# Performance work log

Measured on AMD Instinct MI355X. Metric: run time of the kernel, lower is better.

## Reference

```python
import jax, jax.numpy as jnp
import numpy as np

L, S, D, H, DL, V, B = 8, 1024, 768, 12, 64, 512, 8
NB, NM = 32, 64  # big_bird neighbours, global memory columns


def _bigbird_mask():
    i = np.arange(S)[:, None]
    j = np.arange(S)[None, :]
    m = ((np.abs(i - j) <= NB) | (j < NM)) & (j <= i)  # window + global cols, then tril
    return jnp.asarray(m)[None, None]  # [1,1,S,S]


def _ln(x, g, b):
    mu = x.mean(-1, keepdims=True)
    var = ((x - mu) ** 2).mean(-1, keepdims=True)
    return (x - mu) / jnp.sqrt(var + 1e-5) * g + b


def setup_inputs() -> dict:
    key = jax.random.key(0)
    ks = jax.random.split(key, 16)
    s = 0.02
    d = {
        'x': jax.random.randint(ks[0], (B, S), 0, V),
        'targets': jax.random.randint(ks[1], (B, S), 0, V),
        'wte': jax.random.normal(ks[2], (V, D), jnp.float32) * s,
        'pos': jnp.zeros((1, S, D), jnp.float32),
        'ln1_g': jnp.ones((L, D)), 'ln1_b': jnp.zeros((L, D)),
        'wq': jax.random.normal(ks[3], (L, D, D)) * s, 'bq': jnp.zeros((L, D)),
        'wk': jax.random.normal(ks[4], (L, D, D)) * s, 'bk': jnp.zeros((L, D)),
        'wv': jax.random.normal(ks[5], (L, D, D)) * s, 'bv': jnp.zeros((L, D)),
        'ln2_g': jnp.ones((L, D)), 'ln2_b': jnp.zeros((L, D)),
        'w1': jax.random.normal(ks[6], (L, D, 4 * D)) * s, 'b1': jnp.zeros((L, 4 * D)),
        'w2': jax.random.normal(ks[7], (L, 4 * D, D)) * s, 'b2': jnp.zeros((L, D)),
        'lnf_g': jnp.ones((D,)), 'lnf_b': jnp.zeros((D,)),
        'w_out': jax.random.normal(ks[8], (D, V)) * s,
    }
    return d


def _forward(x, targets, wte, pos, ln1_g, ln1_b, wq, bq, wk, bk, wv, bv,
             ln2_g, ln2_b, w1, b1, w2, b2, lnf_g, lnf_b, w_out):
    mask = _bigbird_mask()
    h = wte[x] + pos  # [B,S,D]
    scale = DL ** -0.5
    neg_inf = jnp.array(float('-inf'), h.dtype)
    for l in range(L):
        a = _ln(h, ln1_g[l], ln1_b[l])
        q = (a @ wq[l] + bq[l]).reshape(B, S, H, DL).transpose(0, 2, 1, 3)
        k = (a @ wk[l] + bk[l]).reshape(B, S, H, DL).transpose(0, 2, 1, 3)
        v = (a @ wv[l] + bv[l]).reshape(B, S, H, DL).transpose(0, 2, 1, 3)
        att = jnp.einsum('bhqd,bhkd->bhqk', q, k) * scale
        att = jnp.where(mask, att, neg_inf)
        att = jax.nn.softmax(att, axis=-1)
        z = jnp.einsum('bhqk,bhkd->bhqd', att, v)
        z = z.transpose(0, 2, 1, 3).reshape(B, S, D)
        h = h + z  # note: W_0 is defined in the torch module but never applied
        m = _ln(h, ln2_g[l], ln2_b[l])
        h = h + jax.nn.gelu(m @ w1[l] + b1[l], approximate=False) @ w2[l] + b2[l]
    h = _ln(h, lnf_g, lnf_b)
    pred = h @ w_out  # [B,S,V]
    logp = jax.nn.log_softmax(pred.reshape(B * S, V), axis=-1)
    loss = -jnp.take_along_axis(logp, targets.reshape(-1, 1), axis=1).mean()
    return pred, loss


def reference(x, targets, wte, pos, ln1_g, ln1_b, wq, bq, wk, bk, wv, bv,
              ln2_g, ln2_b, w1, b1, w2, b2, lnf_g, lnf_b, w_out):
    return _forward(x, targets, wte, pos, ln1_g, ln1_b, wq, bq, wk, bk, wv, bv,
                    ln2_g, ln2_b, w1, b1, w2, b2, lnf_g, lnf_b, w_out)
```

## Files before the change

### kernel.cpp

```cpp
#include <hip/hip_runtime.h>
#include <hip/hip_bf16.h>

#define DEV __device__ __forceinline__

typedef __attribute__((ext_vector_type(8))) short short8;
typedef __attribute__((ext_vector_type(4))) float f32x4;

DEV unsigned short f2bf(float f){
  unsigned int u = __builtin_bit_cast(unsigned int, f);
  u += 0x7FFFu + ((u >> 16) & 1u);
  return (unsigned short)(u >> 16);
}

DEV void gld_lds16(const void* g, void* l){
  __builtin_amdgcn_global_load_lds((const __attribute__((address_space(1))) void*)g,
                                   (__attribute__((address_space(3))) void*)l, 16, 0, 0);
}

__global__ void k_embed(const int* __restrict__ x, const float* __restrict__ wte,
                        const float* __restrict__ pos, float* __restrict__ h){
  int i = blockIdx.x * 256 + threadIdx.x;
  int row = i / 768, d = i - row * 768;
  int s = row & 1023;
  h[i] = wte[x[row] * 768 + d] + pos[s * 768 + d];
}

__global__ void k_ln(const float* __restrict__ src, const float* __restrict__ g,
                     const float* __restrict__ b, unsigned short* __restrict__ out){
  int row = blockIdx.x, t = threadIdx.x;
  const float* p = src + (size_t)row * 768;
  float v0 = p[t], v1 = p[t + 256], v2 = p[t + 512];
  float s = v0 + v1 + v2;
  float sq = v0 * v0 + v1 * v1 + v2 * v2;
  #pragma unroll
  for(int m = 32; m >= 1; m >>= 1){ s += __shfl_xor(s, m); sq += __shfl_xor(sq, m); }
  __shared__ float red[8];
  int w = t >> 6;
  if((t & 63) == 0){ red[w] = s; red[4 + w] = sq; }
  __syncthreads();
  float S  = red[0] + red[1] + red[2] + red[3];
  float SQ = red[4] + red[5] + red[6] + red[7];
  float mu  = S * (1.0f / 768.0f);
  float var = SQ * (1.0f / 768.0f) - mu * mu;
  float inv = rsqrtf(var + 1e-5f);
  unsigned short* o = out + (size_t)row * 768;
  o[t]       = f2bf((v0 - mu) * inv * g[t]       + b[t]);
  o[t + 256] = f2bf((v1 - mu) * inv * g[t + 256] + b[t + 256]);
  o[t + 512] = f2bf((v2 - mu) * inv * g[t + 512] + b[t + 512]);
}

DEV void tr_tile(float (*tl)[33], const float* __restrict__ src, unsigned short* __restrict__ dst,
                 int R, int C, int tx, int ty, int tid){
  int lx = tid & 31, ly = tid >> 5;
  int r0 = ty * 32, c0 = tx * 32;
  #pragma unroll
  for(int i = 0; i < 4; i++) tl[ly + 8*i][lx] = src[(size_t)(r0 + ly + 8*i) * C + (c0 + lx)];
  __syncthreads();
  #pragma unroll
  for(int i = 0; i < 4; i++) dst[(size_t)(c0 + ly + 8*i) * R + (r0 + lx)] = f2bf(tl[lx][ly + 8*i]);
}

__global__ void k_convert_all(const float* __restrict__ wq, const float* __restrict__ wk,
                              const float* __restrict__ wv, const float* __restrict__ w1,
                              const float* __restrict__ w2, const float* __restrict__ bq,
                              const float* __restrict__ bk, const float* __restrict__ bv,
                              unsigned short* __restrict__ wall, float* __restrict__ qkvb,
                              int l0){
  __shared__ float tl[32][33];
  int l = l0 + blockIdx.y, slot = blockIdx.y;
  int bid = blockIdx.x, tid = threadIdx.x;
  unsigned short* wqkv_t = wall + (size_t)slot * 6488064;
  unsigned short* w1_t   = wqkv_t + 1769472;
  unsigned short* w2_t   = w1_t + 2359296;
  float* qb = qkvb + slot * 2304;
  const float* wq_l = wq + (size_t)l * 589824;
  const float* wk_l = wk + (size_t)l * 589824;
  const float* wv_l = wv + (size_t)l * 589824;
  const float* w1_l = w1 + (size_t)l * 2359296;
  const float* w2_l = w2 + (size_t)l * 2359296;
  if(bid < 1728){
    int which = bid / 576, t = bid - which * 576;
    const float* src = which == 0 ? wq_l : which == 1 ? wk_l : wv_l;
    tr_tile(tl, src, wqkv_t + (size_t)which * 589824, 768, 768, t % 24, t / 24, tid);
  } else if(bid < 1728 + 2304){
    int t = bid - 1728;
    tr_tile(tl, w1_l, w1_t, 768, 3072, t % 96, t / 96, tid);
  } else if(bid < 1728 + 4608){
    int t = bid - 4032;
    tr_tile(tl, w2_l, w2_t, 3072, 768, t % 24, t / 24, tid);
  } else {
    for(int i = tid; i < 768; i += 256){
      qb[i] = bq[l * 768 + i]; qb[768 + i] = bk[l * 768 + i]; qb[1536 + i] = bv[l * 768 + i];
    }
  }
}

__global__ void k_transpose(const float* __restrict__ src, unsigned short* __restrict__ dst,
                            int R, int C){
  __shared__ float tl[32][33];
  int nx = C / 32;
  tr_tile(tl, src, dst, R, C, blockIdx.x % nx, blockIdx.x / nx, threadIdx.x);
}

template<int EPI, int NB>
__global__ __launch_bounds__(256)
void k_gemm(const unsigned short* __restrict__ A, const unsigned short* __restrict__ Bt,
            const float* __restrict__ bias, int K,
            float* __restrict__ fout, unsigned short* __restrict__ o0,
            unsigned short* __restrict__ o1, unsigned short* __restrict__ o2){
  __shared__ unsigned short As[128 * 64];
  __shared__ unsigned short Bs[128 * 64];
  int tid = threadIdx.x, w = tid >> 6, lane = tid & 63;
  int nbx = gridDim.x;
  int bid = blockIdx.y * nbx + blockIdx.x;
  int cpx = (nbx * gridDim.y) >> 3;
  int sid = (bid & 7) * cpx + (bid >> 3);
  int bm = sid / nbx, bn = sid - bm * nbx;
  int N = nbx * NB * 32;
  int wr = w >> 1, wc = w & 1;
  f32x4 acc[4][NB] = {};
  int rowA[4], colA[4];
  #pragma unroll
  for(int i = 0; i < 4; i++){
    int o = ((i * 4 + w) << 10) + (lane << 4);
    int r = o >> 7;
    int ch = (o >> 4) & 7;
    rowA[i] = r;
    colA[i] = ((ch ^ (r & 7)) << 3);
  }
  const size_t aBase = (size_t)bm * 128;
  const size_t bBase = (size_t)bn * (NB * 32);
  for(int kt = 0; kt < K; kt += 64){
    #pragma unroll
    for(int i = 0; i < 4; i++)
      gld_lds16(A + (aBase + rowA[i]) * K + kt + colA[i], (char*)As + ((i * 4 + w) << 10));
    #pragma unroll
    for(int i = 0; i < NB; i++)
      gld_lds16(Bt + (bBase + rowA[i]) * K + kt + colA[i], (char*)Bs + ((i * 4 + w) << 10));
    __syncthreads();
    #pragma unroll
    for(int s = 0; s < 2; s++){
      short8 af[4], bfr[NB];
      #pragma unroll
      for(int m = 0; m < 4; m++){
        int r = wr * 64 + m * 16 + (lane & 15);
        int ch = s * 4 + (lane >> 4);
        af[m] = *(const short8*)(As + r * 64 + ((ch ^ (r & 7)) << 3));
      }
      #pragma unroll
      for(int n = 0; n < NB; n++){
        int r = wc * (NB * 16) + n * 16 + (lane & 15);
        int ch = s * 4 + (lane >> 4);
        bfr[n] = *(const short8*)(Bs + r * 64 + ((ch ^ (r & 7)) << 3));
      }
      #pragma unroll
      for(int m = 0; m < 4; m++)
        #pragma unroll
        for(int n = 0; n < NB; n++)
          acc[m][n] = __builtin_amdgcn_mfma_f32_16x16x32_bf16(af[m], bfr[n], acc[m][n], 0, 0, 0);
    }
    __syncthreads();
  }
  int r0 = bm * 128 + wr * 64 + ((lane >> 4) << 2);
  int c0 = bn * (NB * 32) + wc * (NB * 16) + (lane & 15);
  if(EPI == 0){
    unsigned short* dstn[NB];
    float bvn[NB];
    #pragma unroll
    for(int n = 0; n < NB; n++){
      int col = c0 + n * 16;
      bvn[n] = bias[col];
      int which = col / 768, cc = col - which * 768;
      int hd = cc >> 6, dl = cc & 63;
      unsigned short* dst = which == 0 ? o0 : which == 1 ? o1 : o2;
      dstn[n] = dst + (size_t)hd * 65536 + dl;
    }
    #pragma unroll
    for(int m = 0; m < 4; m++){
      #pragma unroll
      for(int j = 0; j < 4; j++){
        int row = r0 + m * 16 + j;
        int bb = row >> 10, sp = row & 1023;
        size_t ro = ((size_t)bb * 12288 + sp) * 64;
        #pragma unroll
        for(int n = 0; n < NB; n++)
          dstn[n][ro] = f2bf(acc[m][n][j] + bvn[n]);
      }
    }
  } else {
    float bvn[NB];
    #pragma unroll
    for(int n = 0; n < NB; n++) bvn[n] = (EPI == 3) ? 0.0f : bias[c0 + n * 16];
    #pragma unroll
    for(int m = 0; m < 4; m++){
      #pragma unroll
      for(int j = 0; j < 4; j++){
        int row = r0 + m * 16 + j;
        #pragma unroll
        for(int n = 0; n < NB; n++){
          int col = c0 + n * 16;
          float v = acc[m][n][j] + bvn[n];
          if(EPI == 1){
            float t = v * (1.5957691f + 0.07135481f * v * v);
            float gl = v * __builtin_amdgcn_rcpf(1.0f + __expf(-t));
            o0[(size_t)row * N + col] = f2bf(gl);
          } else if(EPI == 2){
            fout[(size_t)row * 768 + col] += v;
          } else {
            fout[(size_t)row * 512 + col] = v;
          }
        }
      }
    }
  }
}

__global__ __launch_bounds__(256)
void k_attn(const unsigned short* __restrict__ qg, const unsigned short* __restrict__ kg,
            const unsigned short* __restrict__ vg, float* __restrict__ h){
  __shared__ unsigned short Vt[64 * 256];
  __shared__ unsigned short Ps[4][32 * 128];
  int qb = blockIdx.x, bh = blockIdx.y;
  int tid = threadIdx.x, w = tid >> 6, lane = tid & 63;
  int b = bh / 12, hd = bh - b * 12;
  int wbase = qb * 128 - 32;
  const unsigned short* vb = vg + (size_t)bh * 1024 * 64;
  for(int u = tid; u < 224 * 8; u += 256){
    int slot = u >> 3, c8 = u & 7;
    int j = slot < 64 ? slot : wbase + (slot - 64);
    if(j < 0) j = 0;
    short8 vv = *(const short8*)(vb + (size_t)j * 64 + c8 * 8);
    #pragma unroll
    for(int e = 0; e < 8; e++){
      int d = c8 * 8 + e;
      Vt[d * 256 + (((slot >> 3) ^ (d & 7)) << 3) + (slot & 7)] = (unsigned short)vv[e];
    }
  }
  __syncthreads();
  int i0 = qb * 128 + 32 * w;
  const unsigned short* qrow = qg + (size_t)bh * 1024 * 64;
  const unsigned short* krow = kg + (size_t)bh * 1024 * 64;
  short8 qf[2][2];
  #pragma unroll
  for(int m = 0; m < 2; m++)
    #pragma unroll
    for(int s = 0; s < 2; s++)
      qf[m][s] = *(const short8*)(qrow + (size_t)(i0 + m * 16 + (lane & 15)) * 64 + s * 32 + ((lane >> 4) << 3));
  f32x4 sacc[2][8] = {};
  #pragma unroll
  for(int n = 0; n < 8; n++){
    int jk = (n < 4) ? (n * 16 + (lane & 15))
                     : (wbase + 32 * w + (n - 4) * 16 + (lane & 15));
    int jc = jk < 0 ? 0 : jk;
    const unsigned short* kr = krow + (size_t)jc * 64 + ((lane >> 4) << 3);
    short8 k0 = *(const short8*)(kr);
    short8 k1 = *(const short8*)(kr + 32);
    #pragma unroll
    for(int m = 0; m < 2; m++){
      sacc[m][n] = __builtin_amdgcn_mfma_f32_16x16x32_bf16(qf[m][0], k0, sacc[m][n], 0, 0, 0);
      sacc[m][n] = __builtin_amdgcn_mfma_f32_16x16x32_bf16(qf[m][1], k1, sacc[m][n], 0, 0, 0);
    }
  }
  #pragma unroll
  for(int m = 0; m < 2; m++)
    #pragma unroll
    for(int n = 0; n < 8; n++){
      int s_ = n * 16 + (lane & 15);
      int jkey = (n < 4) ? s_ : (wbase + 32 * w + (s_ - 64));
      #pragma unroll
      for(int j = 0; j < 4; j++){
        int qi = i0 + m * 16 + ((lane >> 4) << 2) + j;
        bool ok = (n < 4) ? (jkey <= qi)
                          : (jkey >= 64 && jkey <= qi && (qi - jkey) <= 32);
        sacc[m][n][j] = ok ? sacc[m][n][j] * 0.125f : -1e30f;
      }
    }
  float rsum[2][4];
  #pragma unroll
  for(int m = 0; m < 2; m++)
    #pragma unroll
    for(int j = 0; j < 4; j++){
      float mx = sacc[m][0][j];
      #pragma unroll
      for(int n = 1; n < 8; n++) mx = fmaxf(mx, sacc[m][n][j]);
      mx = fmaxf(mx, __shfl_xor(mx, 1)); mx = fmaxf(mx, __shfl_xor(mx, 2));
      mx = fmaxf(mx, __shfl_xor(mx, 4)); mx = fmaxf(mx, __shfl_xor(mx, 8));
      float sm = 0.f;
      #pragma unroll
      for(int n = 0; n < 8; n++){
        float e = expf(sacc[m][n][j] - mx);
        sacc[m][n][j] = e;
        sm += e;
      }
      sm += __shfl_xor(sm, 1); sm += __shfl_xor(sm, 2);
      sm += __shfl_xor(sm, 4); sm += __shfl_xor(sm, 8);
      rsum[m][j] = sm;
    }
  unsigned short* Pw = Ps[w];
  #pragma unroll
  for(int m = 0; m < 2; m++)
    #pragma unroll
    for(int n = 0; n < 8; n++){
      int s_ = n * 16 + (lane & 15);
      #pragma unroll
      for(int j = 0; j < 4; j++){
        int ql = m * 16 + ((lane >> 4) << 2) + j;
        Pw[ql * 128 + (((s_ >> 3) ^ (ql & 7)) << 3) + (s_ & 7)] = f2bf(sacc[m][n][j]);
      }
    }
  f32x4 oacc[2][4] = {};
  #pragma unroll
  for(int s = 0; s < 4; s++){
    short8 pa[2];
    #pragma unroll
    for(int m = 0; m < 2; m++){
      int ql = m * 16 + (lane & 15);
      int ch = s * 4 + (lane >> 4);
      pa[m] = *(const short8*)(Pw + ql * 128 + ((ch ^ (ql & 7)) << 3));
    }
    int kk = s * 32 + ((lane >> 4) << 3);
    int slot0 = kk < 64 ? kk : 64 + 32 * w + (kk - 64);
    #pragma unroll
    for(int n = 0; n < 4; n++){
      int d = n * 16 + (lane & 15);
      short8 vv = *(const short8*)(Vt + d * 256 + (((slot0 >> 3) ^ (d & 7)) << 3));
      #pragma unroll
      for(int m = 0; m < 2; m++)
        oacc[m][n] = __builtin_amdgcn_mfma_f32_16x16x32_bf16(pa[m], vv, oacc[m][n], 0, 0, 0);
    }
  }
  #pragma unroll
  for(int m = 0; m < 2; m++)
    #pragma unroll
    for(int j = 0; j < 4; j++){
      int ql = m * 16 + ((lane >> 4) << 2) + j;
      float inv = 1.0f / rsum[m][j];
      size_t base = ((size_t)(b * 1024 + i0 + ql)) * 768 + hd * 64;
      #pragma unroll
      for(int n = 0; n < 4; n++){
        int d = n * 16 + (lane & 15);
        h[base + d] += oacc[m][n][j] * inv;
      }
    }
}

__global__ void k_rowloss(const float* __restrict__ pred, const int* __restrict__ tgt,
                          float* __restrict__ rowloss){
  int row = blockIdx.x * 4 + (threadIdx.x >> 6);
  int lane = threadIdx.x & 63;
  const float* p = pred + (size_t)row * 512 + lane * 8;
  float v[8];
  #pragma unroll
  for(int i = 0; i < 8; i++) v[i] = p[i];
  float mx = v[0];
  #pragma unroll
  for(int i = 1; i < 8; i++) mx = fmaxf(mx, v[i]);
  #pragma unroll
  for(int m = 1; m < 64; m <<= 1) mx = fmaxf(mx, __shfl_xor(mx, m));
  float se = 0.f;
  #pragma unroll
  for(int i = 0; i < 8; i++) se += expf(v[i] - mx);
  #pragma unroll
  for(int m = 1; m < 64; m <<= 1) se += __shfl_xor(se, m);
  int t = tgt[row];
  float pt = 0.f;
  int base = lane * 8;
  #pragma unroll
  for(int i = 0; i < 8; i++) pt = (t == base + i) ? v[i] : pt;
  #pragma unroll
  for(int m = 1; m < 64; m <<= 1) pt += __shfl_xor(pt, m);
  if(lane == 0) rowloss[row] = -(pt - mx - logf(se));
}

__global__ void k_lossfinal(const float* __restrict__ rowloss, float* __restrict__ out){
  int tid = threadIdx.x;
  float s = 0.f;
  for(int i = tid; i < 8192; i += 256) s += rowloss[i];
  #pragma unroll
  for(int m = 32; m >= 1; m >>= 1) s += __shfl_xor(s, m);
  __shared__ float red[4];
  if((tid & 63) == 0) red[tid >> 6] = s;
  __syncthreads();
  if(tid == 0) out[0] = (red[0] + red[1] + red[2] + red[3]) * (1.0f / 8192.0f);
}

extern "C" void kernel_launch(void* const* d_in, const int* in_sizes, int n_in,
                              void* d_out, int out_size, void* d_ws, size_t ws_size,
                              hipStream_t stream){
  const int*   x       = (const int*)d_in[0];
  const int*   targets = (const int*)d_in[1];
  const float* wte     = (const float*)d_in[2];
  const float* pos     = (const float*)d_in[3];
  const float* ln1_g   = (const float*)d_in[4];
  const float* ln1_b   = (const float*)d_in[5];
  const float* wq      = (const float*)d_in[6];
  const float* bq      = (const float*)d_in[7];
  const float* wk      = (const float*)d_in[8];
  const float* bk      = (const float*)d_in[9];
  const float* wv      = (const float*)d_in[10];
  const float* bv      = (const float*)d_in[11];
  const float* ln2_g   = (const float*)d_in[12];
  const float* ln2_b   = (const float*)d_in[13];
  const float* w1      = (const float*)d_in[14];
  const float* b1      = (const float*)d_in[15];
  const float* w2      = (const float*)d_in[16];
  const float* b2      = (const float*)d_in[17];
  const float* lnf_g   = (const float*)d_in[18];
  const float* lnf_b   = (const float*)d_in[19];
  const float* w_out   = (const float*)d_in[20];
  float* out = (float*)d_out;

  char* ws = (char*)d_ws;
  float*          h      = (float*)ws;
  unsigned short* a_bf   = (unsigned short*)(ws + 25165824);
  char*           big    = ws + 37748736;
  unsigned short* qbf    = (unsigned short*)big;
  unsigned short* kbf    = (unsigned short*)(big + 12582912);
  unsigned short* vbf    = (unsigned short*)(big + 25165824);
  unsigned short* tbf    = (unsigned short*)big;
  bool mega = ws_size >= 192782336ull;
  unsigned short* wall   = (unsigned short*)(ws + 88080384);
  size_t wend = 88080384ull + (mega ? 103809024ull : 12976128ull);
  unsigned short* wout_t = (unsigned short*)(ws + wend);
  float*          qkvb   = (float*)(ws + wend + 786432);
  float*          rowls  = (float*)(ws + wend + 786432 + (mega ? 73728 : 9216));

  if(mega)
    k_convert_all<<<dim3(6337, 8), 256, 0, stream>>>(wq, wk, wv, w1, w2, bq, bk, bv,
                                                     wall, qkvb, 0);
  k_transpose<<<384, 256, 0, stream>>>(w_out, wout_t, 768, 512);
  k_embed<<<24576, 256, 0, stream>>>(x, wte, pos, h);
  for(int l = 0; l < 8; l++){
    if(!mega)
      k_convert_all<<<dim3(6337, 1), 256, 0, stream>>>(wq, wk, wv, w1, w2, bq, bk, bv,
                                                       wall, qkvb, l);
    int slot = mega ? l : 0;
    unsigned short* wqkv_l = wall + (size_t)slot * 6488064;
    unsigned short* w1_l   = wqkv_l + 1769472;
    unsigned short* w2_l   = w1_l + 2359296;
    float*          qkvb_l = qkvb + slot * 2304;
    k_ln<<<8192, 256, 0, stream>>>(h, ln1_g + l * 768, ln1_b + l * 768, a_bf);
    k_gemm<0,4><<<dim3(18, 64), 256, 0, stream>>>(a_bf, wqkv_l, qkvb_l, 768, nullptr, qbf, kbf, vbf);
    k_attn<<<dim3(8, 96), 256, 0, stream>>>(qbf, kbf, vbf, h);
    k_ln<<<8192, 256, 0, stream>>>(h, ln2_g + l * 768, ln2_b + l * 768, a_bf);
    k_gemm<1,4><<<dim3(24, 64), 256, 0, stream>>>(a_bf, w1_l, b1 + l * 3072, 768, nullptr, tbf, nullptr, nullptr);
    k_gemm<2,2><<<dim3(12, 64), 256, 0, stream>>>(tbf, w2_l, b2 + l * 768, 3072, h, nullptr, nullptr, nullptr);
  }
  k_ln<<<8192, 256, 0, stream>>>(h, lnf_g, lnf_b, a_bf);
  k_gemm<3,2><<<dim3(8, 64), 256, 0, stream>>>(a_bf, wout_t, nullptr, 768, out, nullptr, nullptr, nullptr);
  k_rowloss<<<2048, 256, 0, stream>>>(out, targets, rowls);
  k_lossfinal<<<1, 256, 0, stream>>>(rowls, out + 4194304);
}
```

Before: 1.619 ms.

## Use 256-row GEMM tiles with 8 warps and 64-row weight transposes

Templates the GEMM on warp-rows (MW), so the QKV and FC1 GEMMs run 512-thread blocks covering 256 rows each, sharing each B tile across more A rows and halving the grid. The weight-transpose kernels now handle 64x32 tiles and write packed bf16 pairs as 32-bit stores, halving block count and store instructions. The larger blocks double LDS for A and add register pressure under the new launch-bounds occupancy hint, which may reduce concurrent blocks per CU.

Result: no change. 1.595 ms (-1.5%).

```diff
diff --git a/kernel.cpp b/kernel.cpp
--- a/kernel.cpp
+++ b/kernel.cpp
@@ -49,15 +49,21 @@
   o[t + 512] = f2bf((v2 - mu) * inv * g[t + 512] + b[t + 512]);
 }
 
-DEV void tr_tile(float (*tl)[33], const float* __restrict__ src, unsigned short* __restrict__ dst,
-                 int R, int C, int tx, int ty, int tid){
+DEV void tr_tile64(float (*tl)[33], const float* __restrict__ src, unsigned short* __restrict__ dst,
+                   int R, int C, int tx, int ty, int tid){
   int lx = tid & 31, ly = tid >> 5;
-  int r0 = ty * 32, c0 = tx * 32;
-  #pragma unroll
-  for(int i = 0; i < 4; i++) tl[ly + 8*i][lx] = src[(size_t)(r0 + ly + 8*i) * C + (c0 + lx)];
+  int r0 = ty * 64, c0 = tx * 32;
+  #pragma unroll
+  for(int i = 0; i < 8; i++)
+    tl[ly + 8 * i][lx] = src[(size_t)(r0 + ly + 8 * i) * C + (c0 + lx)];
   __syncthreads();
   #pragma unroll
-  for(int i = 0; i < 4; i++) dst[(size_t)(c0 + ly + 8*i) * R + (r0 + lx)] = f2bf(tl[lx][ly + 8*i]);
+  for(int j = 0; j < 4; j++){
+    int oc = ly + 8 * j;
+    unsigned int pk = (unsigned int)f2bf(tl[2 * lx][oc]) |
+                      ((unsigned int)f2bf(tl[2 * lx + 1][oc]) << 16);
+    *(unsigned int*)(dst + (size_t)(c0 + oc) * R + r0 + 2 * lx) = pk;
+  }
 }
 
 __global__ void k_convert_all(const float* __restrict__ wq, const float* __restrict__ wk,
@@ -66,7 +72,7 @@
                               const float* __restrict__ bk, const float* __restrict__ bv,
                               unsigned short* __restrict__ wall, float* __restrict__ qkvb,
                               int l0){
-  __shared__ float tl[32][33];
+  __shared__ float tl[64][33];
   int l = l0 + blockIdx.y, slot = blockIdx.y;
   int bid = blockIdx.x, tid = threadIdx.x;
   unsigned short* wqkv_t = wall + (size_t)slot * 6488064;
@@ -78,16 +84,16 @@
   const float* wv_l = wv + (size_t)l * 589824;
   const float* w1_l = w1 + (size_t)l * 2359296;
   const float* w2_l = w2 + (size_t)l * 2359296;
-  if(bid < 1728){
-    int which = bid / 576, t = bid - which * 576;
+  if(bid < 864){
+    int which = bid / 288, t = bid - which * 288;
     const float* src = which == 0 ? wq_l : which == 1 ? wk_l : wv_l;
-    tr_tile(tl, src, wqkv_t + (size_t)which * 589824, 768, 768, t % 24, t / 24, tid);
-  } else if(bid < 1728 + 2304){
-    int t = bid - 1728;
-    tr_tile(tl, w1_l, w1_t, 768, 3072, t % 96, t / 96, tid);
-  } else if(bid < 1728 + 4608){
-    int t = bid - 4032;
-    tr_tile(tl, w2_l, w2_t, 3072, 768, t % 24, t / 24, tid);
+    tr_tile64(tl, src, wqkv_t + (size_t)which * 589824, 768, 768, t % 24, t / 24, tid);
+  } else if(bid < 864 + 1152){
+    int t = bid - 864;
+    tr_tile64(tl, w1_l, w1_t, 768, 3072, t % 96, t / 96, tid);
+  } else if(bid < 864 + 2304){
+    int t = bid - 2016;
+    tr_tile64(tl, w2_l, w2_t, 3072, 768, t % 24, t / 24, tid);
   } else {
     for(int i = tid; i < 768; i += 256){
       qb[i] = bq[l * 768 + i]; qb[768 + i] = bk[l * 768 + i]; qb[1536 + i] = bv[l * 768 + i];
@@ -97,20 +103,24 @@
 
 __global__ void k_transpose(const float* __restrict__ src, unsigned short* __restrict__ dst,
                             int R, int C){
-  __shared__ float tl[32][33];
+  __shared__ float tl[64][33];
   int nx = C / 32;
-  tr_tile(tl, src, dst, R, C, blockIdx.x % nx, blockIdx.x / nx, threadIdx.x);
-}
-
-template<int EPI, int NB>
-__global__ __launch_bounds__(256)
+  tr_tile64(tl, src, dst, R, C, blockIdx.x % nx, blockIdx.x / nx, threadIdx.x);
+}
+
+template<int EPI, int MW, int NB>
+__global__ __launch_bounds__(MW * 128, 4)
 void k_gemm(const unsigned short* __restrict__ A, const unsigned short* __restrict__ Bt,
             const float* __restrict__ bias, int K,
             float* __restrict__ fout, unsigned short* __restrict__ o0,
             unsigned short* __restrict__ o1, unsigned short* __restrict__ o2){
-  __shared__ unsigned short As[128 * 64];
-  __shared__ unsigned short Bs[128 * 64];
+  constexpr int THREADS = MW * 128;
+  constexpr int AL = 4;
+  constexpr int BL = (2 * NB) / MW;
+  __shared__ unsigned short As[MW * 64 * 64];
+  __shared__ unsigned short Bs[NB * 32 * 64];
   int tid = threadIdx.x, w = tid >> 6, lane = tid & 63;
+  int l15 = lane & 15, l4 = lane >> 4;
   int nbx = gridDim.x;
   int bid = blockIdx.y * nbx + blockIdx.x;
   int cpx = (nbx * gridDim.y) >> 3;
@@ -119,38 +129,44 @@
   int N = nbx * NB * 32;
   int wr = w >> 1, wc = w & 1;
   f32x4 acc[4][NB] = {};
-  int rowA[4], colA[4];
-  #pragma unroll
-  for(int i = 0; i < 4; i++){
-    int o = ((i * 4 + w) << 10) + (lane << 4);
-    int r = o >> 7;
-    int ch = (o >> 4) & 7;
-    rowA[i] = r;
-    colA[i] = ((ch ^ (r & 7)) << 3);
-  }
-  const size_t aBase = (size_t)bm * 128;
+  int rowA[AL], colA[AL], rowB[BL], colB[BL];
+  #pragma unroll
+  for(int i = 0; i < AL; i++){
+    int o = i * THREADS * 16 + tid * 16;
+    int r = o >> 7, ch = (o >> 4) & 7;
+    rowA[i] = r; colA[i] = ((ch ^ (r & 7)) << 3);
+  }
+  #pragma unroll
+  for(int i = 0; i < BL; i++){
+    int o = i * THREADS * 16 + tid * 16;
+    int r = o >> 7, ch = (o >> 4) & 7;
+    rowB[i] = r; colB[i] = ((ch ^ (r & 7)) << 3);
+  }
+  const size_t aBase = (size_t)bm * (MW * 64);
   const size_t bBase = (size_t)bn * (NB * 32);
   for(int kt = 0; kt < K; kt += 64){
     #pragma unroll
-    for(int i = 0; i < 4; i++)
-      gld_lds16(A + (aBase + rowA[i]) * K + kt + colA[i], (char*)As + ((i * 4 + w) << 10));
-    #pragma unroll
-    for(int i = 0; i < NB; i++)
-      gld_lds16(Bt + (bBase + rowA[i]) * K + kt + colA[i], (char*)Bs + ((i * 4 + w) << 10));
+    for(int i = 0; i < AL; i++)
+      gld_lds16(A + (aBase + rowA[i]) * K + kt + colA[i],
+                (char*)As + i * THREADS * 16 + tid * 16);
+    #pragma unroll
+    for(int i = 0; i < BL; i++)
+      gld_lds16(Bt + (bBase + rowB[i]) * K + kt + colB[i],
+                (char*)Bs + i * THREADS * 16 + tid * 16);
     __syncthreads();
     #pragma unroll
     for(int s = 0; s < 2; s++){
       short8 af[4], bfr[NB];
       #pragma unroll
       for(int m = 0; m < 4; m++){
-        int r = wr * 64 + m * 16 + (lane & 15);
-        int ch = s * 4 + (lane >> 4);
+        int r = wr * 64 + m * 16 + l15;
+        int ch = s * 4 + l4;
         af[m] = *(const short8*)(As + r * 64 + ((ch ^ (r & 7)) << 3));
       }
       #pragma unroll
       for(int n = 0; n < NB; n++){
-        int r = wc * (NB * 16) + n * 16 + (lane & 15);
-        int ch = s * 4 + (lane >> 4);
+        int r = wc * (NB * 16) + n * 16 + l15;
+        int ch = s * 4 + l4;
         bfr[n] = *(const short8*)(Bs + r * 64 + ((ch ^ (r & 7)) << 3));
       }
       #pragma unroll
@@ -161,8 +177,8 @@
     }
     __syncthreads();
   }
-  int r0 = bm * 128 + wr * 64 + ((lane >> 4) << 2);
-  int c0 = bn * (NB * 32) + wc * (NB * 16) + (lane & 15);
+  int r0 = bm * (MW * 64) + wr * 64 + (l4 << 2);
+  int c0 = bn * (NB * 32) + wc * (NB * 16) + l15;
   if(EPI == 0){
     unsigned short* dstn[NB];
     float bvn[NB];
@@ -426,13 +442,13 @@
   float*          rowls  = (float*)(ws + wend + 786432 + (mega ? 73728 : 9216));
 
   if(mega)
-    k_convert_all<<<dim3(6337, 8), 256, 0, stream>>>(wq, wk, wv, w1, w2, bq, bk, bv,
+    k_convert_all<<<dim3(3169, 8), 256, 0, stream>>>(wq, wk, wv, w1, w2, bq, bk, bv,
                                                      wall, qkvb, 0);
-  k_transpose<<<384, 256, 0, stream>>>(w_out, wout_t, 768, 512);
+  k_transpose<<<192, 256, 0, stream>>>(w_out, wout_t, 768, 512);
   k_embed<<<24576, 256, 0, stream>>>(x, wte, pos, h);
   for(int l = 0; l < 8; l++){
     if(!mega)
-      k_convert_all<<<dim3(6337, 1), 256, 0, stream>>>(wq, wk, wv, w1, w2, bq, bk, bv,
+      k_convert_all<<<dim3(3169, 1), 256, 0, stream>>>(wq, wk, wv, w1, w2, bq, bk, bv,
                                                        wall, qkvb, l);
     int slot = mega ? l : 0;
     unsigned short* wqkv_l = wall + (size_t)slot * 6488064;
@@ -440,14 +456,14 @@
     unsigned short* w2_l   = w1_l + 2359296;
     float*          qkvb_l = qkvb + slot * 2304;
     k_ln<<<8192, 256, 0, stream>>>(h, ln1_g + l * 768, ln1_b + l * 768, a_bf);
-    k_gemm<0,4><<<dim3(18, 64), 256, 0, stream>>>(a_bf, wqkv_l, qkvb_l, 768, nullptr, qbf, kbf, vbf);
+    k_gemm<0,4,4><<<dim3(18, 32), 512, 0, stream>>>(a_bf, wqkv_l, qkvb_l, 768, nullptr, qbf, kbf, vbf);
     k_attn<<<dim3(8, 96), 256, 0, stream>>>(qbf, kbf, vbf, h);
     k_ln<<<8192, 256, 0, stream>>>(h, ln2_g + l * 768, ln2_b + l * 768, a_bf);
-    k_gemm<1,4><<<dim3(24, 64), 256, 0, stream>>>(a_bf, w1_l, b1 + l * 3072, 768, nullptr, tbf, nullptr, nullptr);
-    k_gemm<2,2><<<dim3(12, 64), 256, 0, stream>>>(tbf, w2_l, b2 + l * 768, 3072, h, nullptr, nullptr, nullptr);
+    k_gemm<1,4,4><<<dim3(24, 32), 512, 0, stream>>>(a_bf, w1_l, b1 + l * 3072, 768, nullptr, tbf, nullptr, nullptr);
+    k_gemm<2,2,2><<<dim3(12, 64), 256, 0, stream>>>(tbf, w2_l, b2 + l * 768, 3072, h, nullptr, nullptr, nullptr);
   }
   k_ln<<<8192, 256, 0, stream>>>(h, lnf_g, lnf_b, a_bf);
-  k_gemm<3,2><<<dim3(8, 64), 256, 0, stream>>>(a_bf, wout_t, nullptr, 768, out, nullptr, nullptr, nullptr);
+  k_gemm<3,2,2><<<dim3(8, 64), 256, 0, stream>>>(a_bf, wout_t, nullptr, 768, out, nullptr, nullptr, nullptr);
   k_rowloss<<<2048, 256, 0, stream>>>(out, targets, rowls);
   k_lossfinal<<<1, 256, 0, stream>>>(rowls, out + 4194304);
 }
```
